# Optimization experiments

Measured on AMD Instinct MI355X. Metric: run time of the kernel, lower is better.

Reference implementation:

```python
import jax, jax.numpy as jnp
import numpy as np

PATCH = 4
EPS = 1e-6
B, C_IN, HW = 4, 32, 256


def _avg_pool(x, k):
    # x: (B, C, H, W) -> (B, C, H//k, W//k), mean over kxk non-overlapping patches
    b, c, h, w = x.shape
    return x.reshape(b, c, h // k, k, w // k, k).mean(axis=(3, 5))


def _shift(x, dr, dc):
    # y[r, c] = x[r+dr, c+dc] if in-bounds else 0 (|dr|,|dc| <= 1); x: (B, H, W)
    xp = jnp.pad(x, ((0, 0), (1, 1), (1, 1)))
    h, w = x.shape[1], x.shape[2]
    return xp[:, 1 + dr:1 + dr + h, 1 + dc:1 + dc + w]


def setup_inputs() -> dict:
    key = jax.random.key(0)
    k1, k2 = jax.random.split(key)
    x_feat = jax.random.normal(k1, (B, C_IN, HW, HW), dtype=jnp.float32)
    x_var = jax.random.uniform(k2, (B, 1, HW, HW), dtype=jnp.float32)  # uncertainty in [0,1]
    return {"x_feat": x_feat, "x_var": x_var}


def reference(x_feat, x_var):
    # F.interpolate(x_var, size=x_feat.shape[-2:]) is identity here (same spatial size).
    xv = 1.0 - _avg_pool(x_var, PATCH)[:, 0]          # (B, H, W) patch certainty
    pooled = _avg_pool(x_feat, PATCH)                  # (B, C, H, W)
    # ones (C,C,kh,kw) conv kernel: every output channel = sum over input channels of patch mean
    xf = jnp.broadcast_to(pooled.sum(axis=1, keepdims=True), pooled.shape)  # (B, C, H, W)
    b, c, h, w = xf.shape
    n = h * w
    # torch .view(-1, C) on a (C,H,W) tensor: raw row-major reshape, not a transpose
    nodes = xf.reshape(b, n, c)                        # (B, N, C)

    r, cc = jnp.meshgrid(jnp.arange(h), jnp.arange(w), indexing="ij")
    to_flat = (r * w + cc).reshape(-1)                 # (N,) destination node ids
    adj = jnp.zeros((b, n, n), dtype=xv.dtype)         # dense form of sparse_coo edge weights

    # direction -> dir_shift used by EdgeChecker (y[pos] = x[pos + shift])
    for dr, dc in ((1, 0), (-1, 0), (0, 1), (0, -1)):  # up, down, left, right
        d = _shift(xv, dr, dc) - xv                    # (B, H, W) neighbor - self
        valid = (r + dr >= 0) & (r + dr < h) & (cc + dc >= 0) & (cc + dc < w)
        wgt = jnp.where((d > EPS) & valid, d, 0.0).reshape(b, -1)  # (B, N)
        from_flat = jnp.where(valid, (r + dr) * w + (cc + dc), 0).reshape(-1)  # (N,)
        adj = adj.at[:, from_flat, to_flat].add(wgt)

    return nodes, adj
```

## Files before the change

### kernel.cpp

```cpp
#include <hip/hip_runtime.h>

#define HW    256
#define PH    64
#define PW    64
#define CIN   32
#define NB    4
#define NNODE 4096
#define EPS_W 1e-6f

__global__ __launch_bounds__(256) void pool_kernel(
    const float* __restrict__ x_feat, const float* __restrict__ x_var,
    float* __restrict__ S, float* __restrict__ XV) {
    const int blk  = blockIdx.x;
    const int b    = blk >> 6;
    const int r    = blk & 63;
    const int lane = threadIdx.x & 63;
    const int wave = threadIdx.x >> 6;

    __shared__ float red[256];

    float acc = 0.f;
    #pragma unroll
    for (int c = 0; c < 8; ++c) {
        const int ch = wave * 8 + c;
        const float4* p =
            (const float4*)(x_feat + (((size_t)(b * CIN + ch) * HW + r * 4) * HW)) + lane;
        #pragma unroll
        for (int pr = 0; pr < 4; ++pr) {
            float4 v = p[pr * (HW / 4)];
            acc += v.x + v.y + v.z + v.w;
        }
    }
    red[threadIdx.x] = acc;
    __syncthreads();

    if (wave == 0) {
        float s = red[lane] + red[lane + 64] + red[lane + 128] + red[lane + 192];
        S[(b << 12) + (r << 6) + lane] = s * (1.0f / 16.0f);
    } else if (wave == 1) {
        const float4* p = (const float4*)(x_var + ((size_t)b * HW + r * 4) * HW) + lane;
        float a = 0.f;
        #pragma unroll
        for (int pr = 0; pr < 4; ++pr) {
            float4 v = p[pr * (HW / 4)];
            a += v.x + v.y + v.z + v.w;
        }
        XV[(b << 12) + (r << 6) + lane] = 1.0f - a * (1.0f / 16.0f);
    }
}

__global__ __launch_bounds__(256) void nodes_kernel(
    const float* __restrict__ S, float* __restrict__ out) {
    const int i = blockIdx.x * blockDim.x + threadIdx.x;
    const int b = i >> 15;
    const int g = i & 32767;
    float4 v = ((const float4*)S)[(b << 10) + (g & 1023)];
    ((float4*)out)[i] = v;
}

__global__ __launch_bounds__(256) void scatter_kernel(
    const float* __restrict__ XV, float* __restrict__ adj) {
    const int i   = blockIdx.x * blockDim.x + threadIdx.x;
    const int b   = i >> 12;
    const int pos = i & 4095;
    const int r   = pos >> 6;
    const int c   = pos & 63;

    const float  self = XV[i];
    const float* xvb  = XV + (b << 12);
    float*       A    = adj + (size_t)b * NNODE * NNODE;

    if (r + 1 < PH) {
        float d = xvb[pos + 64] - self;
        if (d > EPS_W) A[(size_t)(pos + 64) * NNODE + pos] = d;
    }
    if (r - 1 >= 0) {
        float d = xvb[pos - 64] - self;
        if (d > EPS_W) A[(size_t)(pos - 64) * NNODE + pos] = d;
    }
    if (c + 1 < PW) {
        float d = xvb[pos + 1] - self;
        if (d > EPS_W) A[(size_t)(pos + 1) * NNODE + pos] = d;
    }
    if (c - 1 >= 0) {
        float d = xvb[pos - 1] - self;
        if (d > EPS_W) A[(size_t)(pos - 1) * NNODE + pos] = d;
    }
}

extern "C" void kernel_launch(void* const* d_in, const int* in_sizes, int n_in,
                              void* d_out, int out_size, void* d_ws, size_t ws_size,
                              hipStream_t stream) {
    const float* x_feat = (const float*)d_in[0];
    const float* x_var  = (const float*)d_in[1];
    float* out = (float*)d_out;

    float* S  = (float*)d_ws;
    float* XV = S + NB * NNODE;

    hipMemsetAsync(d_out, 0, (size_t)out_size * sizeof(float), stream);

    pool_kernel<<<NB * PH, 256, 0, stream>>>(x_feat, x_var, S, XV);
    nodes_kernel<<<512, 256, 0, stream>>>(S, out);
    scatter_kernel<<<64, 256, 0, stream>>>(XV, out + (size_t)NB * CIN * NNODE);
}
```

Measured before the change: 294.7 us.

## Fuse adjacency zero-fill with edge computation into one dense nontemporal-store kernel

Removes the full-output memset and the sparse scatter kernel. A single dense kernel now writes every float4 of the adjacency matrix, computing the neighbor weight inline for the few entries near the diagonal band and zero elsewhere, using nontemporal stores. This avoids a separate zeroing pass and a scattered write pass over the 256 MB output, at the cost of a large grid and per-element index checks.

Measured after the change: 284.4 us. 1.04x faster.

```diff
diff --git a/kernel.cpp b/kernel.cpp
--- a/kernel.cpp
+++ b/kernel.cpp
@@ -7,6 +7,8 @@
 #define NB    4
 #define NNODE 4096
 #define EPS_W 1e-6f
+
+typedef float f32x4 __attribute__((ext_vector_type(4)));
 
 __global__ __launch_bounds__(256) void pool_kernel(
     const float* __restrict__ x_feat, const float* __restrict__ x_var,
@@ -58,34 +60,33 @@
     ((float4*)out)[i] = v;
 }
 
-__global__ __launch_bounds__(256) void scatter_kernel(
+__global__ __launch_bounds__(256) void adj_kernel(
     const float* __restrict__ XV, float* __restrict__ adj) {
-    const int i   = blockIdx.x * blockDim.x + threadIdx.x;
-    const int b   = i >> 12;
-    const int pos = i & 4095;
-    const int r   = pos >> 6;
-    const int c   = pos & 63;
+    const int i    = blockIdx.x * blockDim.x + threadIdx.x;
+    const int b    = i >> 22;
+    const int rem  = i & 4194303;
+    const int from = rem >> 10;
+    const int c0   = (rem & 1023) << 2;
 
-    const float  self = XV[i];
-    const float* xvb  = XV + (b << 12);
-    float*       A    = adj + (size_t)b * NNODE * NNODE;
+    f32x4 v = (f32x4)(0.f);
 
-    if (r + 1 < PH) {
-        float d = xvb[pos + 64] - self;
-        if (d > EPS_W) A[(size_t)(pos + 64) * NNODE + pos] = d;
+    if (c0 >= from - 67 && c0 <= from + 64) {
+        const float* xvb = XV + (b << 12);
+        const float  xvf = xvb[from];
+        #pragma unroll
+        for (int j = 0; j < 4; ++j) {
+            const int col = c0 + j;
+            const int d   = from - col;
+            const bool nb = (d == 64) | (d == -64) |
+                            ((d == 1)  & ((from & 63) != 0)) |
+                            ((d == -1) & ((from & 63) != 63));
+            if (nb) {
+                float diff = xvf - xvb[col];
+                v[j] = diff > EPS_W ? diff : 0.f;
+            }
+        }
     }
-    if (r - 1 >= 0) {
-        float d = xvb[pos - 64] - self;
-        if (d > EPS_W) A[(size_t)(pos - 64) * NNODE + pos] = d;
-    }
-    if (c + 1 < PW) {
-        float d = xvb[pos + 1] - self;
-        if (d > EPS_W) A[(size_t)(pos + 1) * NNODE + pos] = d;
-    }
-    if (c - 1 >= 0) {
-        float d = xvb[pos - 1] - self;
-        if (d > EPS_W) A[(size_t)(pos - 1) * NNODE + pos] = d;
-    }
+    __builtin_nontemporal_store(v, (f32x4*)adj + i);
 }
 
 extern "C" void kernel_launch(void* const* d_in, const int* in_sizes, int n_in,
@@ -98,9 +99,7 @@
     float* S  = (float*)d_ws;
     float* XV = S + NB * NNODE;
 
-    hipMemsetAsync(d_out, 0, (size_t)out_size * sizeof(float), stream);
-
     pool_kernel<<<NB * PH, 256, 0, stream>>>(x_feat, x_var, S, XV);
     nodes_kernel<<<512, 256, 0, stream>>>(S, out);
-    scatter_kernel<<<64, 256, 0, stream>>>(XV, out + (size_t)NB * CIN * NNODE);
+    adj_kernel<<<65536, 256, 0, stream>>>(XV, out + (size_t)NB * CIN * NNODE);
 }
```
